# Performance work log

Measured on AMD Instinct MI355X. Metric: run time of the kernel, lower is better.

## Reference

```python
import jax, jax.numpy as jnp
import numpy as np

K_DIM = 1024
HEADS = 16


def setup_inputs() -> dict:
    key = jax.random.key(0)
    ks = jax.random.split(key, 6)
    b, t, k = 2, 2048, K_DIM
    scale = 1.0 / np.sqrt(k)
    x = jax.random.normal(ks[0], (b, t, k), dtype=jnp.float32)
    # nn.Linear stores weight as [out, in]; y = x @ W.T
    Wq = jax.random.normal(ks[1], (k, k), dtype=jnp.float32) * scale
    Wk = jax.random.normal(ks[2], (k, k), dtype=jnp.float32) * scale
    Wv = jax.random.normal(ks[3], (k, k), dtype=jnp.float32) * scale
    Wo = jax.random.normal(ks[4], (k, k), dtype=jnp.float32) * scale
    bo = jax.random.normal(ks[5], (k,), dtype=jnp.float32) * scale
    return {"x": x, "Wq": Wq, "Wk": Wk, "Wv": Wv, "Wo": Wo, "bo": bo}


def reference(x, Wq, Wk, Wv, Wo, bo):
    b, t, k = x.shape
    h = HEADS
    hd = k // h
    q = (x @ Wq.T).reshape(b, t, h, hd)
    kk = (x @ Wk.T).reshape(b, t, h, hd)
    v = (x @ Wv.T).reshape(b, t, h, hd)
    # scores: [b, h, t, t]
    scores = jnp.einsum('bqhd,bkhd->bhqk', q, kk) / jnp.sqrt(jnp.float32(hd))
    w = jax.nn.softmax(scores, axis=-1)
    out = jnp.einsum('bhqk,bkhd->bqhd', w, v).reshape(b, t, k)
    return out @ Wo.T + bo
```

## Files before the change

### kernel.cpp

```cpp
#include <hip/hip_runtime.h>
#include <stdint.h>
#include <stddef.h>

#define TB 2048
#define KDIM 1024
#define NH 16
#define HD 64

typedef __attribute__((ext_vector_type(8))) __bf16 bf16x8;
typedef __attribute__((ext_vector_type(4))) float f32x4;
typedef __attribute__((ext_vector_type(16))) float f32x16;
typedef __attribute__((ext_vector_type(8))) unsigned short u16x8;
typedef __attribute__((ext_vector_type(4))) unsigned u32x4;
typedef __attribute__((ext_vector_type(2))) unsigned u32x2;

static __device__ __forceinline__ unsigned short f2bf(float f) {
  unsigned u = __builtin_bit_cast(unsigned, f);
  return (unsigned short)((u + 0x7FFFu + ((u >> 16) & 1u)) >> 16);
}

static __device__ __forceinline__ bf16x8 ld_frag(const unsigned short* p) {
  u16x8 v = *(const u16x8*)p;
  return __builtin_bit_cast(bf16x8, v);
}

static __device__ __forceinline__ void gload_lds16(const void* g, void* l) {
  auto gp = (const __attribute__((address_space(1))) unsigned int*)(uintptr_t)g;
  auto lp = (__attribute__((address_space(3))) unsigned int*)(unsigned int)(uintptr_t)l;
  __builtin_amdgcn_global_load_lds(gp, lp, 16, 0, 0);
}

static __device__ __forceinline__ float fast_exp2(float x) {
  float r;
  asm("v_exp_f32 %0, %1" : "=v"(r) : "v"(x));
  return r;
}

static __device__ __forceinline__ unsigned cvt_pk(float a, float b) {
  unsigned r;
  asm("v_cvt_pk_bf16_f32 %0, %1, %2" : "=v"(r) : "v"(a), "v"(b));
  return r;
}

static __device__ __forceinline__ u32x2 permswap(unsigned a, unsigned b) {
  return __builtin_amdgcn_permlane32_swap(a, b, false, false);
}

__global__ __launch_bounds__(256) void k_cvt_all(
    const float* __restrict__ x, const float* __restrict__ Wq,
    const float* __restrict__ Wk, const float* __restrict__ Wv,
    const float* __restrict__ Wo, unsigned short* __restrict__ xb,
    unsigned short* __restrict__ wb) {
  int bb = blockIdx.x;
  const float* src;
  unsigned short* dst;
  int i;
  if (bb < 2048) {
    src = x; dst = xb; i = bb * 256 + threadIdx.x;
  } else {
    int wsel = (bb - 2048) >> 9;
    src = (wsel == 0) ? Wq : (wsel == 1) ? Wk : (wsel == 2) ? Wv : Wo;
    dst = wb + (size_t)wsel * (KDIM * KDIM);
    i = ((bb - 2048) & 511) * 256 + threadIdx.x;
  }
  const float4* p = (const float4*)src + (size_t)i * 2;
  float4 a = p[0], b = p[1];
  u16x8 o;
  o[0] = f2bf(a.x); o[1] = f2bf(a.y); o[2] = f2bf(a.z); o[3] = f2bf(a.w);
  o[4] = f2bf(b.x); o[5] = f2bf(b.y); o[6] = f2bf(b.z); o[7] = f2bf(b.w);
  *((u16x8*)dst + i) = o;
}

template <int MODE>
static __device__ __forceinline__ void gemm_body(
    const unsigned short* __restrict__ A, const unsigned short* __restrict__ W,
    unsigned short* __restrict__ Cb, float* __restrict__ Cf,
    const float* __restrict__ bias, int by, int bx,
    unsigned short* As, unsigned short* Bs) {
  const int K = KDIM, N = KDIM;
  int tid = threadIdx.x, lane = tid & 63, wid = tid >> 6;
  int r = lane & 15, g = lane >> 4;
  int wm = wid >> 1, wn = wid & 1;

  f32x4 acc[4][4];
#pragma unroll
  for (int m = 0; m < 4; ++m)
#pragma unroll
    for (int n = 0; n < 4; ++n) acc[m][n] = (f32x4){0.f, 0.f, 0.f, 0.f};

  const unsigned short* Ag = A + (size_t)(by * 128) * K;
  const unsigned short* Wg = W + (size_t)(bx * 128) * K;

  for (int k0 = 0; k0 < K; k0 += 32) {
#pragma unroll
    for (int it = 0; it < 2; ++it) {
      int base = it * 256 + wid * 64;
      int c = base + lane;
      gload_lds16(Ag + (size_t)(c >> 2) * K + k0 + (c & 3) * 8, &As[base * 8]);
      gload_lds16(Wg + (size_t)(c >> 2) * K + k0 + (c & 3) * 8, &Bs[base * 8]);
    }
    __syncthreads();
    bf16x8 af[4], bf[4];
#pragma unroll
    for (int m = 0; m < 4; ++m) af[m] = ld_frag(&As[(wm * 64 + m * 16 + r) * 32 + g * 8]);
#pragma unroll
    for (int n = 0; n < 4; ++n) bf[n] = ld_frag(&Bs[(wn * 64 + n * 16 + r) * 32 + g * 8]);
#pragma unroll
    for (int m = 0; m < 4; ++m)
#pragma unroll
      for (int n = 0; n < 4; ++n)
        acc[m][n] = __builtin_amdgcn_mfma_f32_16x16x32_bf16(af[m], bf[n], acc[m][n], 0, 0, 0);
    __syncthreads();
  }

#pragma unroll
  for (int m = 0; m < 4; ++m)
#pragma unroll
    for (int n = 0; n < 4; ++n) {
      int col = bx * 128 + wn * 64 + n * 16 + r;
#pragma unroll
      for (int j = 0; j < 4; ++j) {
        int row = by * 128 + wm * 64 + m * 16 + g * 4 + j;
        if (MODE == 0)
          Cb[(size_t)row * N + col] = f2bf(acc[m][n][j]);
        else
          Cf[(size_t)row * N + col] = acc[m][n][j] + bias[col];
      }
    }
}

__global__ __launch_bounds__(256) void k_gemm_qkv(
    const unsigned short* __restrict__ X,
    const unsigned short* __restrict__ Wq, const unsigned short* __restrict__ Wk,
    const unsigned short* __restrict__ Wv,
    unsigned short* __restrict__ Q, unsigned short* __restrict__ Kp,
    unsigned short* __restrict__ V) {
  __shared__ __align__(16) unsigned short As[4096];
  __shared__ __align__(16) unsigned short Bs[4096];
  int idx = blockIdx.x;
  int by = idx / 24, bxx = idx % 24;
  int which = bxx >> 3, bx = bxx & 7;
  const unsigned short* W = (which == 0) ? Wq : (which == 1) ? Wk : Wv;
  unsigned short* C = (which == 0) ? Q : (which == 1) ? Kp : V;
  gemm_body<0>(X, W, C, nullptr, nullptr, by, bx, As, Bs);
}

__global__ __launch_bounds__(256) void k_gemm_out(
    const unsigned short* __restrict__ AO, const unsigned short* __restrict__ Wo,
    float* __restrict__ out, const float* __restrict__ bias) {
  __shared__ __align__(16) unsigned short As[4096];
  __shared__ __align__(16) unsigned short Bs[4096];
  int by = blockIdx.x >> 3, bx = blockIdx.x & 7;
  gemm_body<1>(AO, Wo, nullptr, out, bias, by, bx, As, Bs);
}

__global__ __launch_bounds__(256) void k_transpose_v(
    const unsigned short* __restrict__ V, unsigned short* __restrict__ Vt) {
  int tt = blockIdx.x & 31, bh = blockIdx.x >> 5;
  int b = bh >> 4, h = bh & 15;
  __shared__ __align__(16) unsigned short ls[64][72];
  int tid = threadIdx.x;
#pragma unroll
  for (int it = 0; it < 2; ++it) {
    int c = it * 256 + tid;
    int t = c >> 3, d0 = (c & 7) * 8;
    const unsigned short* src = V + ((size_t)(b * TB + tt * 64 + t)) * KDIM + h * HD + d0;
    *(u16x8*)&ls[t][d0] = *(const u16x8*)src;
  }
  __syncthreads();
#pragma unroll
  for (int it = 0; it < 2; ++it) {
    int c = it * 256 + tid;
    int d = c >> 3, t0 = (c & 7) * 8;
    u16x8 v;
#pragma unroll
    for (int j = 0; j < 8; ++j) v[j] = ls[t0 + j][d];
    unsigned short* dst = Vt + ((size_t)(bh * HD + d)) * TB + tt * 64 + t0;
    *(u16x8*)dst = v;
  }
}

__global__ __launch_bounds__(512, 4) void k_attn(
    const unsigned short* __restrict__ Q, const unsigned short* __restrict__ Kp,
    const unsigned short* __restrict__ Vt, unsigned short* __restrict__ AO) {
  __shared__ __align__(16) unsigned short Ks[2][2][4096];
  __shared__ __align__(16) unsigned short Vs[2][2][4096];

  int qt = blockIdx.x & 15, bh = blockIdx.x >> 4;
  int b = bh >> 4, h = bh & 15;
  int tid = threadIdx.x, lane = tid & 63, w = tid >> 6;
  int wl = w & 3, half = w >> 2;
  int q = lane & 31, hh = lane >> 5;
  const float LOG2E = 1.44269504f;
  const int HT = (TB / 64) / 2;

  const unsigned short* Qp =
      Q + ((size_t)(b * TB + qt * 128 + wl * 32 + q)) * KDIM + h * HD;
  bf16x8 qf[4];
#pragma unroll
  for (int f = 0; f < 4; ++f) qf[f] = ld_frag(&Qp[16 * f + 8 * hh]);

  f32x16 o0, o1;
#pragma unroll
  for (int i = 0; i < 16; ++i) { o0[i] = 0.f; o1[i] = 0.f; }
  float m_run = -1e30f, l_run = 0.f;

  const unsigned short* Kbase = Kp + (size_t)(b * TB) * KDIM + h * HD;
  const unsigned short* Vbase = Vt + (size_t)bh * HD * TB;

  auto stage = [&](int kt, int buf) {
#pragma unroll
    for (int it = 0; it < 2; ++it) {
      int base = it * 256 + wl * 64;
      int c = base + lane;
      int rr = c >> 3;
      int blk = (c & 7) ^ (rr & 7);
      gload_lds16(Kbase + (size_t)(kt * 64 + rr) * KDIM + blk * 8,
                  &Ks[half][buf][base * 8]);
      gload_lds16(Vbase + (size_t)rr * TB + kt * 64 + blk * 8,
                  &Vs[half][buf][base * 8]);
    }
  };

  stage(half * HT, 0);
  __syncthreads();
  int cur = 0;

  for (int t = 0; t < HT; ++t) {
    if (t + 1 < HT) stage(half * HT + t + 1, cur ^ 1);

    const unsigned short* Kc = &Ks[half][cur][0];
    f32x16 st[2];
    __builtin_amdgcn_s_setprio(1);
#pragma unroll
    for (int g = 0; g < 2; ++g) {
#pragma unroll
      for (int i = 0; i < 16; ++i) st[g][i] = 0.f;
#pragma unroll
      for (int f = 0; f < 4; ++f) {
        int row = g * 32 + q;
        int bl = (2 * f + hh) ^ (row & 7);
        bf16x8 kf = ld_frag(&Kc[row * 64 + bl * 8]);
        st[g] = __builtin_amdgcn_mfma_f32_32x32x16_bf16(kf, qf[f], st[g], 0, 0, 0);
      }
    }
    __builtin_amdgcn_s_setprio(0);

    float pm4[4] = {-1e30f, -1e30f, -1e30f, -1e30f};
#pragma unroll
    for (int g = 0; g < 2; ++g)
#pragma unroll
      for (int i = 0; i < 16; ++i) pm4[i & 3] = fmaxf(pm4[i & 3], st[g][i]);
    float pm = fmaxf(fmaxf(pm4[0], pm4[1]), fmaxf(pm4[2], pm4[3]));
    pm = fmaxf(pm, __shfl_xor(pm, 32));
    float spm = pm * 0.125f;
    if (!__all(spm <= m_run + 8.f)) {
      float mnew = fmaxf(m_run, spm);
      float sc = fast_exp2((m_run - mnew) * LOG2E);
      m_run = mnew;
      l_run *= sc;
#pragma unroll
      for (int p = 0; p < 16; ++p) {
        float scp = __shfl(sc, (p & 3) + 8 * (p >> 2) + 4 * hh);
        o0[p] *= scp;
        o1[p] *= scp;
      }
    }

    float c1 = 0.125f * LOG2E, c2 = m_run * LOG2E;
    float rs4[4] = {0.f, 0.f, 0.f, 0.f};
    bf16x8 pa[4];
#pragma unroll
    for (int g = 0; g < 2; ++g) {
      float e[16];
#pragma unroll
      for (int i = 0; i < 16; ++i) {
        e[i] = fast_exp2(st[g][i] * c1 - c2);
        rs4[i & 3] += e[i];
      }
      unsigned d[8];
#pragma unroll
      for (int i = 0; i < 8; ++i) d[i] = cvt_pk(e[2 * i], e[2 * i + 1]);
      u32x2 r1 = permswap(d[0], d[2]);
      u32x2 r2 = permswap(d[1], d[3]);
      u32x2 r3 = permswap(d[4], d[6]);
      u32x2 r4 = permswap(d[5], d[7]);
      u32x4 t0; t0[0] = r1.x; t0[1] = r2.x; t0[2] = r1.y; t0[3] = r2.y;
      u32x4 t1; t1[0] = r3.x; t1[1] = r4.x; t1[2] = r3.y; t1[3] = r4.y;
      pa[2 * g]     = __builtin_bit_cast(bf16x8, t0);
      pa[2 * g + 1] = __builtin_bit_cast(bf16x8, t1);
    }
    float rs = (rs4[0] + rs4[1]) + (rs4[2] + rs4[3]);
    rs += __shfl_xor(rs, 32);
    l_run += rs;

    const unsigned short* Vc = &Vs[half][cur][0];
    __builtin_amdgcn_s_setprio(1);
#pragma unroll
    for (int s = 0; s < 4; ++s) {
      int bl = (2 * s + hh) ^ (q & 7);
      bf16x8 v0 = ld_frag(&Vc[q * 64 + bl * 8]);
      bf16x8 v1 = ld_frag(&Vc[(32 + q) * 64 + bl * 8]);
      o0 = __builtin_amdgcn_mfma_f32_32x32x16_bf16(pa[s], v0, o0, 0, 0, 0);
      o1 = __builtin_amdgcn_mfma_f32_32x32x16_bf16(pa[s], v1, o1, 0, 0, 0);
    }
    __builtin_amdgcn_s_setprio(0);

    __syncthreads();
    cur ^= 1;
  }

  float* Osw = (float*)&Vs[0][0][0];
  float* MLb = (float*)&Ks[0][0][0];
  if (half) {
#pragma unroll
    for (int p = 0; p < 16; ++p) {
      Osw[p * 256 + wl * 64 + lane]        = o0[p];
      Osw[(16 + p) * 256 + wl * 64 + lane] = o1[p];
    }
    if (!hh) {
      MLb[wl * 32 + q]       = m_run;
      MLb[128 + wl * 32 + q] = l_run;
    }
  }
  __syncthreads();
  if (!half) {
    float m2 = MLb[wl * 32 + q], l2 = MLb[128 + wl * 32 + q];
    float mm = fmaxf(m_run, m2);
    float ea = fast_exp2((m_run - mm) * LOG2E);
    float eb = fast_exp2((m2 - mm) * LOG2E);
    float il = 1.f / (l_run * ea + l2 * eb);
#pragma unroll
    for (int p = 0; p < 16; ++p) {
      int qr = (p & 3) + 8 * (p >> 2) + 4 * hh;
      float a  = __shfl(ea, qr);
      float bb = __shfl(eb, qr);
      float ip = __shfl(il, qr);
      float v0 = (o0[p] * a + Osw[p * 256 + wl * 64 + lane] * bb) * ip;
      float v1 = (o1[p] * a + Osw[(16 + p) * 256 + wl * 64 + lane] * bb) * ip;
      int row = qt * 128 + wl * 32 + qr;
      size_t base = ((size_t)(b * TB + row)) * KDIM + h * HD;
      AO[base + q]      = f2bf(v0);
      AO[base + 32 + q] = f2bf(v1);
    }
  }
}

extern "C" void kernel_launch(void* const* d_in, const int* in_sizes, int n_in,
                              void* d_out, int out_size, void* d_ws, size_t ws_size,
                              hipStream_t stream) {
  const float* x  = (const float*)d_in[0];
  const float* Wq = (const float*)d_in[1];
  const float* Wk = (const float*)d_in[2];
  const float* Wv = (const float*)d_in[3];
  const float* Wo = (const float*)d_in[4];
  const float* bo = (const float*)d_in[5];

  char* ws = (char*)d_ws;
  const size_t MB = 1 << 20;
  unsigned short* xb  = (unsigned short*)(ws + 0 * MB);
  unsigned short* wqb = (unsigned short*)(ws + 8 * MB);
  unsigned short* wkb = (unsigned short*)(ws + 10 * MB);
  unsigned short* wvb = (unsigned short*)(ws + 12 * MB);
  unsigned short* wob = (unsigned short*)(ws + 14 * MB);
  unsigned short* Qb  = (unsigned short*)(ws + 16 * MB);
  unsigned short* Kb  = (unsigned short*)(ws + 24 * MB);
  unsigned short* Vb  = (unsigned short*)(ws + 32 * MB);
  unsigned short* Vtb = (unsigned short*)(ws + 40 * MB);
  unsigned short* AOb = (unsigned short*)(ws + 48 * MB);

  k_cvt_all<<<4096, 256, 0, stream>>>(x, Wq, Wk, Wv, Wo, xb, wqb);
  k_gemm_qkv<<<32 * 24, 256, 0, stream>>>(xb, wqb, wkb, wvb, Qb, Kb, Vb);
  k_transpose_v<<<1024, 256, 0, stream>>>(Vb, Vtb);
  k_attn<<<512, 512, 0, stream>>>(Qb, Kb, Vtb, AOb);
  k_gemm_out<<<256, 256, 0, stream>>>(AOb, wob, (float*)d_out, bo);
}
```

Before: 125.5 us.

## Fuse V transpose into QKV GEMM, widen GEMM K-tile with swizzle, pack softmax math

The V projection now writes its output directly in the transposed [b,h,d,t] layout from the GEMM epilogue, so the separate transpose kernel and its extra round trip through memory are gone. The GEMM K step grows from 32 to 64, with an XOR-swizzled LDS layout to avoid bank conflicts and MFMA priority hints. The attention softmax uses max3 reductions and packed FMA/add instructions to cut VALU work. The larger LDS tiles may reduce occupancy, and the transposed V stores are narrow 8-byte strided writes.

```diff
diff --git a/kernel.cpp b/kernel.cpp
--- a/kernel.cpp
+++ b/kernel.cpp
@@ -8,8 +8,10 @@
 #define HD 64
 
 typedef __attribute__((ext_vector_type(8))) __bf16 bf16x8;
+typedef __attribute__((ext_vector_type(2))) float f32x2;
 typedef __attribute__((ext_vector_type(4))) float f32x4;
 typedef __attribute__((ext_vector_type(16))) float f32x16;
+typedef __attribute__((ext_vector_type(4))) unsigned short u16x4;
 typedef __attribute__((ext_vector_type(8))) unsigned short u16x8;
 typedef __attribute__((ext_vector_type(4))) unsigned u32x4;
 typedef __attribute__((ext_vector_type(2))) unsigned u32x2;
@@ -44,6 +46,22 @@
 
 static __device__ __forceinline__ u32x2 permswap(unsigned a, unsigned b) {
   return __builtin_amdgcn_permlane32_swap(a, b, false, false);
+}
+
+static __device__ __forceinline__ f32x2 pk_fma(f32x2 a, f32x2 b, f32x2 c) {
+  f32x2 d;
+  asm("v_pk_fma_f32 %0, %1, %2, %3" : "=v"(d) : "v"(a), "v"(b), "v"(c));
+  return d;
+}
+static __device__ __forceinline__ f32x2 pk_add(f32x2 a, f32x2 b) {
+  f32x2 d;
+  asm("v_pk_add_f32 %0, %1, %2" : "=v"(d) : "v"(a), "v"(b));
+  return d;
+}
+static __device__ __forceinline__ float max3f(float a, float b, float c) {
+  float d;
+  asm("v_max3_f32 %0, %1, %2, %3" : "=v"(d) : "v"(a), "v"(b), "v"(c));
+  return d;
 }
 
 __global__ __launch_bounds__(256) void k_cvt_all(
@@ -91,25 +109,38 @@
   const unsigned short* Ag = A + (size_t)(by * 128) * K;
   const unsigned short* Wg = W + (size_t)(bx * 128) * K;
 
-  for (int k0 = 0; k0 < K; k0 += 32) {
-#pragma unroll
-    for (int it = 0; it < 2; ++it) {
+  for (int k0 = 0; k0 < K; k0 += 64) {
+#pragma unroll
+    for (int it = 0; it < 4; ++it) {
       int base = it * 256 + wid * 64;
       int c = base + lane;
-      gload_lds16(Ag + (size_t)(c >> 2) * K + k0 + (c & 3) * 8, &As[base * 8]);
-      gload_lds16(Wg + (size_t)(c >> 2) * K + k0 + (c & 3) * 8, &Bs[base * 8]);
+      int rr = c >> 3;
+      int blk = (c & 7) ^ (rr & 7);
+      gload_lds16(Ag + (size_t)rr * K + k0 + blk * 8, &As[base * 8]);
+      gload_lds16(Wg + (size_t)rr * K + k0 + blk * 8, &Bs[base * 8]);
     }
     __syncthreads();
-    bf16x8 af[4], bf[4];
-#pragma unroll
-    for (int m = 0; m < 4; ++m) af[m] = ld_frag(&As[(wm * 64 + m * 16 + r) * 32 + g * 8]);
-#pragma unroll
-    for (int n = 0; n < 4; ++n) bf[n] = ld_frag(&Bs[(wn * 64 + n * 16 + r) * 32 + g * 8]);
-#pragma unroll
-    for (int m = 0; m < 4; ++m)
-#pragma unroll
-      for (int n = 0; n < 4; ++n)
-        acc[m][n] = __builtin_amdgcn_mfma_f32_16x16x32_bf16(af[m], bf[n], acc[m][n], 0, 0, 0);
+#pragma unroll
+    for (int ks = 0; ks < 2; ++ks) {
+      bf16x8 af[4], bf[4];
+#pragma unroll
+      for (int m = 0; m < 4; ++m) {
+        int row = wm * 64 + m * 16 + r;
+        af[m] = ld_frag(&As[row * 64 + ((ks * 4 + g) ^ (r & 7)) * 8]);
+      }
+#pragma unroll
+      for (int n = 0; n < 4; ++n) {
+        int row = wn * 64 + n * 16 + r;
+        bf[n] = ld_frag(&Bs[row * 64 + ((ks * 4 + g) ^ (r & 7)) * 8]);
+      }
+      __builtin_amdgcn_s_setprio(1);
+#pragma unroll
+      for (int m = 0; m < 4; ++m)
+#pragma unroll
+        for (int n = 0; n < 4; ++n)
+          acc[m][n] = __builtin_amdgcn_mfma_f32_16x16x32_bf16(af[m], bf[n], acc[m][n], 0, 0, 0);
+      __builtin_amdgcn_s_setprio(0);
+    }
     __syncthreads();
   }
 
@@ -118,13 +149,23 @@
 #pragma unroll
     for (int n = 0; n < 4; ++n) {
       int col = bx * 128 + wn * 64 + n * 16 + r;
-#pragma unroll
-      for (int j = 0; j < 4; ++j) {
-        int row = by * 128 + wm * 64 + m * 16 + g * 4 + j;
-        if (MODE == 0)
-          Cb[(size_t)row * N + col] = f2bf(acc[m][n][j]);
-        else
-          Cf[(size_t)row * N + col] = acc[m][n][j] + bias[col];
+      if (MODE == 2) {
+        int hq = col >> 6, dq = col & 63;
+        int row0 = by * 128 + wm * 64 + m * 16 + g * 4;
+        int bq = row0 >> 11, tq = row0 & 2047;
+        u16x4 pv;
+#pragma unroll
+        for (int j = 0; j < 4; ++j) pv[j] = f2bf(acc[m][n][j]);
+        *(u16x4*)&Cb[(((size_t)(bq * NH + hq)) * HD + dq) * TB + tq] = pv;
+      } else {
+#pragma unroll
+        for (int j = 0; j < 4; ++j) {
+          int row = by * 128 + wm * 64 + m * 16 + g * 4 + j;
+          if (MODE == 0)
+            Cb[(size_t)row * N + col] = f2bf(acc[m][n][j]);
+          else
+            Cf[(size_t)row * N + col] = acc[m][n][j] + bias[col];
+        }
       }
     }
 }
@@ -134,50 +175,28 @@
     const unsigned short* __restrict__ Wq, const unsigned short* __restrict__ Wk,
     const unsigned short* __restrict__ Wv,
     unsigned short* __restrict__ Q, unsigned short* __restrict__ Kp,
-    unsigned short* __restrict__ V) {
-  __shared__ __align__(16) unsigned short As[4096];
-  __shared__ __align__(16) unsigned short Bs[4096];
+    unsigned short* __restrict__ Vt) {
+  __shared__ __align__(16) unsigned short As[8192];
+  __shared__ __align__(16) unsigned short Bs[8192];
   int idx = blockIdx.x;
   int by = idx / 24, bxx = idx % 24;
   int which = bxx >> 3, bx = bxx & 7;
-  const unsigned short* W = (which == 0) ? Wq : (which == 1) ? Wk : Wv;
-  unsigned short* C = (which == 0) ? Q : (which == 1) ? Kp : V;
-  gemm_body<0>(X, W, C, nullptr, nullptr, by, bx, As, Bs);
+  if (which == 2) {
+    gemm_body<2>(X, Wv, Vt, nullptr, nullptr, by, bx, As, Bs);
+  } else {
+    const unsigned short* W = which ? Wk : Wq;
+    unsigned short* C = which ? Kp : Q;
+    gemm_body<0>(X, W, C, nullptr, nullptr, by, bx, As, Bs);
+  }
 }
 
 __global__ __launch_bounds__(256) void k_gemm_out(
     const unsigned short* __restrict__ AO, const unsigned short* __restrict__ Wo,
     float* __restrict__ out, const float* __restrict__ bias) {
-  __shared__ __align__(16) unsigned short As[4096];
-  __shared__ __align__(16) unsigned short Bs[4096];
+  __shared__ __align__(16) unsigned short As[8192];
+  __shared__ __align__(16) unsigned short Bs[8192];
   int by = blockIdx.x >> 3, bx = blockIdx.x & 7;
   gemm_body<1>(AO, Wo, nullptr, out, bias, by, bx, As, Bs);
-}
-
-__global__ __launch_bounds__(256) void k_transpose_v(
-    const unsigned short* __restrict__ V, unsigned short* __restrict__ Vt) {
-  int tt = blockIdx.x & 31, bh = blockIdx.x >> 5;
-  int b = bh >> 4, h = bh & 15;
-  __shared__ __align__(16) unsigned short ls[64][72];
-  int tid = threadIdx.x;
-#pragma unroll
-  for (int it = 0; it < 2; ++it) {
-    int c = it * 256 + tid;
-    int t = c >> 3, d0 = (c & 7) * 8;
-    const unsigned short* src = V + ((size_t)(b * TB + tt * 64 + t)) * KDIM + h * HD + d0;
-    *(u16x8*)&ls[t][d0] = *(const u16x8*)src;
-  }
-  __syncthreads();
-#pragma unroll
-  for (int it = 0; it < 2; ++it) {
-    int c = it * 256 + tid;
-    int d = c >> 3, t0 = (c & 7) * 8;
-    u16x8 v;
-#pragma unroll
-    for (int j = 0; j < 8; ++j) v[j] = ls[t0 + j][d];
-    unsigned short* dst = Vt + ((size_t)(bh * HD + d)) * TB + tt * 64 + t0;
-    *(u16x8*)dst = v;
-  }
 }
 
 __global__ __launch_bounds__(512, 4) void k_attn(
@@ -246,12 +265,21 @@
     }
     __builtin_amdgcn_s_setprio(0);
 
-    float pm4[4] = {-1e30f, -1e30f, -1e30f, -1e30f};
-#pragma unroll
-    for (int g = 0; g < 2; ++g)
-#pragma unroll
-      for (int i = 0; i < 16; ++i) pm4[i & 3] = fmaxf(pm4[i & 3], st[g][i]);
-    float pm = fmaxf(fmaxf(pm4[0], pm4[1]), fmaxf(pm4[2], pm4[3]));
+    float m0 = max3f(st[0][0], st[0][1], st[0][2]);
+    float m1 = max3f(st[0][3], st[0][4], st[0][5]);
+    float m2 = max3f(st[0][6], st[0][7], st[0][8]);
+    float m3 = max3f(st[0][9], st[0][10], st[0][11]);
+    float m4 = max3f(st[0][12], st[0][13], st[0][14]);
+    float m5 = max3f(st[0][15], st[1][0], st[1][1]);
+    float m6 = max3f(st[1][2], st[1][3], st[1][4]);
+    float m7 = max3f(st[1][5], st[1][6], st[1][7]);
+    float m8 = max3f(st[1][8], st[1][9], st[1][10]);
+    float m9 = max3f(st[1][11], st[1][12], st[1][13]);
+    float u0 = max3f(m0, m1, m2);
+    float u1 = max3f(m3, m4, m5);
+    float u2 = max3f(m6, m7, m8);
+    float u3 = max3f(m9, st[1][14], st[1][15]);
+    float pm = fmaxf(fmaxf(u0, u1), fmaxf(u2, u3));
     pm = fmaxf(pm, __shfl_xor(pm, 32));
     float spm = pm * 0.125f;
     if (!__all(spm <= m_run + 8.f)) {
@@ -268,19 +296,21 @@
     }
 
     float c1 = 0.125f * LOG2E, c2 = m_run * LOG2E;
-    float rs4[4] = {0.f, 0.f, 0.f, 0.f};
+    f32x2 c1v; c1v[0] = c1; c1v[1] = c1;
+    f32x2 c2v; c2v[0] = -c2; c2v[1] = -c2;
+    f32x2 rsv; rsv[0] = 0.f; rsv[1] = 0.f;
     bf16x8 pa[4];
 #pragma unroll
     for (int g = 0; g < 2; ++g) {
-      float e[16];
-#pragma unroll
-      for (int i = 0; i < 16; ++i) {
-        e[i] = fast_exp2(st[g][i] * c1 - c2);
-        rs4[i & 3] += e[i];
-      }
       unsigned d[8];
 #pragma unroll
-      for (int i = 0; i < 8; ++i) d[i] = cvt_pk(e[2 * i], e[2 * i + 1]);
+      for (int i = 0; i < 8; ++i) {
+        f32x2 p; p[0] = st[g][2 * i]; p[1] = st[g][2 * i + 1];
+        p = pk_fma(p, c1v, c2v);
+        f32x2 e; e[0] = fast_exp2(p[0]); e[1] = fast_exp2(p[1]);
+        rsv = pk_add(rsv, e);
+        d[i] = cvt_pk(e[0], e[1]);
+      }
       u32x2 r1 = permswap(d[0], d[2]);
       u32x2 r2 = permswap(d[1], d[3]);
       u32x2 r3 = permswap(d[4], d[6]);
@@ -290,7 +320,7 @@
       pa[2 * g]     = __builtin_bit_cast(bf16x8, t0);
       pa[2 * g + 1] = __builtin_bit_cast(bf16x8, t1);
     }
-    float rs = (rs4[0] + rs4[1]) + (rs4[2] + rs4[3]);
+    float rs = rsv[0] + rsv[1];
     rs += __shfl_xor(rs, 32);
     l_run += rs;
 
@@ -325,10 +355,10 @@
   }
   __syncthreads();
   if (!half) {
-    float m2 = MLb[wl * 32 + q], l2 = MLb[128 + wl * 32 + q];
-    float mm = fmaxf(m_run, m2);
+    float m2r = MLb[wl * 32 + q], l2 = MLb[128 + wl * 32 + q];
+    float mm = fmaxf(m_run, m2r);
     float ea = fast_exp2((m_run - mm) * LOG2E);
-    float eb = fast_exp2((m2 - mm) * LOG2E);
+    float eb = fast_exp2((m2r - mm) * LOG2E);
     float il = 1.f / (l_run * ea + l2 * eb);
 #pragma unroll
     for (int p = 0; p < 16; ++p) {
@@ -365,13 +395,11 @@
   unsigned short* wob = (unsigned short*)(ws + 14 * MB);
   unsigned short* Qb  = (unsigned short*)(ws + 16 * MB);
   unsigned short* Kb  = (unsigned short*)(ws + 24 * MB);
-  unsigned short* Vb  = (unsigned short*)(ws + 32 * MB);
-  unsigned short* Vtb = (unsigned short*)(ws + 40 * MB);
-  unsigned short* AOb = (unsigned short*)(ws + 48 * MB);
+  unsigned short* Vtb = (unsigned short*)(ws + 32 * MB);
+  unsigned short* AOb = (unsigned short*)(ws + 40 * MB);
 
   k_cvt_all<<<4096, 256, 0, stream>>>(x, Wq, Wk, Wv, Wo, xb, wqb);
-  k_gemm_qkv<<<32 * 24, 256, 0, stream>>>(xb, wqb, wkb, wvb, Qb, Kb, Vb);
-  k_transpose_v<<<1024, 256, 0, stream>>>(Vb, Vtb);
+  k_gemm_qkv<<<32 * 24, 256, 0, stream>>>(xb, wqb, wkb, wvb, Qb, Kb, Vtb);
   k_attn<<<512, 512, 0, stream>>>(Qb, Kb, Vtb, AOb);
   k_gemm_out<<<256, 256, 0, stream>>>(AOb, wob, (float*)d_out, bo);
 }
```

Result: faster. 120.2 us (-4.2%).
